# Optimization experiments

Measured on AMD Instinct MI355X. Metric: run time of the kernel, lower is better.

## Reference

```python
import jax, jax.numpy as jnp
import numpy as np

STRIDE = (1, 1, 1)  # (h_stride, w_stride, d_stride)
# padding order in module: (left,right,up,down,forward,backward) -> h, w, d dims
PAD = ((1, 1), (1, 1), (1, 1))  # ((pad_left,pad_right) on h, (up,down) on w, (fwd,bwd) on d)


def setup_inputs() -> dict:
    key = jax.random.key(0)
    k1, k2, k3 = jax.random.split(key, 3)
    X = jax.random.normal(k1, (4, 32, 32, 64, 64), dtype=jnp.float32)        # (B, Cin, h, w, d)
    weight = jax.random.normal(k2, (64, 32, 3, 3, 3), dtype=jnp.float32) * 0.5  # (Cout, Cin, kh, kw, kd)
    bias = jax.random.normal(k3, (64,), dtype=jnp.float32) * 0.5
    return {"X": X, "weight": weight, "bias": bias}


def _conv3d(X, weight, bias):
    # cross-correlation conv3d, identical math to the nested-loop MAC in MyConv3d
    y = jax.lax.conv_general_dilated(
        X, weight,
        window_strides=STRIDE,
        padding=PAD,
        dimension_numbers=("NCHWD", "OIHWD", "NCHWD"),
    )
    return y + bias[None, :, None, None, None]


def reference(X, weight, bias):
    return _conv3d(X, weight, bias)
```

## Files before the change

### kernel.cpp

```cpp
#include <hip/hip_runtime.h>
#include <hip/hip_bf16.h>

typedef __attribute__((ext_vector_type(8))) short bf16x8;
typedef __attribute__((ext_vector_type(4))) float f32x4;

#define B_N   4
#define C_IN  32
#define C_OUT 64
#define S_H   32
#define S_W   64
#define S_D   64
#define HWD   (S_H * S_W * S_D)

#define WPK_USHORTS     (4 * 28 * 64 * 8)
#define WS_NEEDED       ((size_t)WPK_USHORTS * 2 + 64)

__device__ __forceinline__ ushort f2bf(float f) {
    unsigned u = __builtin_bit_cast(unsigned, f);
    unsigned r = (u + 0x7FFFu + ((u >> 16) & 1u)) >> 16;
    return (ushort)r;
}

typedef const __attribute__((address_space(1))) unsigned int* dma_gptr;
typedef __attribute__((address_space(3))) unsigned int* dma_lptr;

__device__ __forceinline__ void dma16(const void* g, void* l) {
    __builtin_amdgcn_global_load_lds((dma_gptr)g, (dma_lptr)l, 16, 0, 0);
}

__device__ __forceinline__ void pin_load(float& dst, const float* p) {
    asm volatile("global_load_dword %0, %1, off" : "=v"(dst) : "v"(p));
}

__global__ __launch_bounds__(256) void pack_w_kernel(
    const float* __restrict__ Wt, ushort* __restrict__ Wpk, float* __restrict__ Zpf)
{
    int idx = blockIdx.x * 256 + threadIdx.x;
    int cic = idx / 1792;
    int r   = idx - cic * 1792;
    int tap = r >> 6;
    int co  = r & 63;
    bf16x8 pk;
    #pragma unroll
    for (int j = 0; j < 8; ++j)
        pk[j] = (tap < 27) ? (short)f2bf(Wt[((long)co * C_IN + cic * 8 + j) * 27 + tap])
                           : (short)0;
    *((bf16x8*)Wpk + idx) = pk;
    if (blockIdx.x == 0 && threadIdx.x < 16) Zpf[threadIdx.x] = 0.f;
}

__global__ __launch_bounds__(256, 2) void conv3d_fused_kernel(
    const float* __restrict__ X, const ushort* __restrict__ Wpk,
    const float* __restrict__ Zpf,
    const float* __restrict__ bias, float* __restrict__ out)
{
    __shared__ ushort Xs[1188 * 8];
    __shared__ ushort Ws[1792 * 8];

    const int tid  = threadIdx.x;
    const int lane = tid & 63;
    const int wave = tid >> 6;
    const int nl   = lane & 15;
    const int quad = lane >> 4;

    const int blk = blockIdx.x;
    const int wt  = blk & 15;
    const int h   = (blk >> 4) & 31;
    const int b   = blk >> 9;
    const int w0  = wt * 4;

    const float* xb[5];
    int adv[5];
    #pragma unroll
    for (int k = 0; k < 5; ++k) {
        int s = tid + k * 256;
        xb[k] = Zpf; adv[k] = 0;
        if (s < 1188) {
            int hh   = s / 396;
            int r0   = s - hh * 396;
            int ww   = r0 / 66;
            int dpos = r0 - ww * 66;
            int hp  = h - 1 + hh;
            int wp2 = w0 - 1 + ww;
            int dp  = dpos - 1;
            bool ok = (unsigned)hp < S_H && (unsigned)wp2 < S_W && (unsigned)dp < S_D;
            if (ok) {
                xb[k]  = X + ((((long)b * C_IN) * S_H + hp) * S_W + wp2) * S_D + dp;
                adv[k] = HWD;
            }
        }
    }

    int a_off[7], b_off[7];
    #pragma unroll
    for (int tg = 0; tg < 7; ++tg) {
        int tap = tg * 4 + quad;
        int tb  = tap < 27 ? tap : 0;
        int kh = tb / 9;
        int r9 = tb - kh * 9;
        int kw = r9 / 3;
        int kd = r9 - kw * 3;
        a_off[tg] = (tap * 64 + nl) * 8;
        b_off[tg] = (((kh * 6 + kw + wave) * 66) + kd + nl) * 8;
    }

    float bs[16];
    #pragma unroll
    for (int mi = 0; mi < 4; ++mi)
        #pragma unroll
        for (int r = 0; r < 4; ++r)
            bs[mi * 4 + r] = bias[mi * 16 + quad * 4 + r];

    f32x4 acc[16];
    #pragma unroll
    for (int i = 0; i < 16; ++i) acc[i] = (f32x4){0.f, 0.f, 0.f, 0.f};

    float xv[5][8];

    #pragma unroll
    for (int k = 0; k < 5; ++k) {
        int s = tid + k * 256;
        if (s < 1188) {
            #pragma unroll
            for (int j = 0; j < 8; ++j)
                pin_load(xv[k][j], xb[k] + (long)j * adv[k]);
        }
    }
    __builtin_amdgcn_sched_barrier(0);
    #pragma unroll
    for (int k = 0; k < 7; ++k) {
        int s = tid + k * 256;
        dma16(Wpk + s * 8, &Ws[s * 8]);
    }
    __builtin_amdgcn_sched_barrier(0);
    asm volatile("s_waitcnt vmcnt(7)" ::: "memory");
    __builtin_amdgcn_sched_barrier(0);
    #pragma unroll
    for (int k = 0; k < 5; ++k) {
        int s = tid + k * 256;
        if (s < 1188) {
            bf16x8 pk;
            #pragma unroll
            for (int j = 0; j < 8; ++j) pk[j] = (short)f2bf(xv[k][j]);
            *(bf16x8*)&Xs[s * 8] = pk;
        }
    }

    for (int cic = 0; cic < 4; ++cic) {
        __syncthreads();

        if (cic < 3) {
            #pragma unroll
            for (int k = 0; k < 5; ++k) {
                int s = tid + k * 256;
                if (s < 1188) {
                    #pragma unroll
                    for (int j = 0; j < 8; ++j)
                        pin_load(xv[k][j],
                                 xb[k] + (long)((cic + 1) * 8 + j) * adv[k]);
                }
            }
        }
        __builtin_amdgcn_sched_barrier(0);

        #pragma unroll
        for (int tg = 0; tg < 7; ++tg) {
            bf16x8 af[4], bf[4];
            #pragma unroll
            for (int mi = 0; mi < 4; ++mi)
                af[mi] = *(const bf16x8*)&Ws[a_off[tg] + mi * 128];
            #pragma unroll
            for (int dt = 0; dt < 4; ++dt)
                bf[dt] = *(const bf16x8*)&Xs[b_off[tg] + dt * 128];
            #pragma unroll
            for (int mi = 0; mi < 4; ++mi)
                #pragma unroll
                for (int dt = 0; dt < 4; ++dt)
                    acc[mi * 4 + dt] = __builtin_amdgcn_mfma_f32_16x16x32_bf16(
                        af[mi], bf[dt], acc[mi * 4 + dt], 0, 0, 0);
        }

        if (cic < 3) {
            __syncthreads();
            asm volatile("s_waitcnt vmcnt(0)" ::: "memory");
            __builtin_amdgcn_sched_barrier(0);

            {
                const ushort* src = Wpk + (long)(cic + 1) * 1792 * 8;
                #pragma unroll
                for (int k = 0; k < 7; ++k) {
                    int s = tid + k * 256;
                    dma16(src + s * 8, &Ws[s * 8]);
                }
            }
            #pragma unroll
            for (int k = 0; k < 5; ++k) {
                int s = tid + k * 256;
                if (s < 1188) {
                    bf16x8 pk;
                    #pragma unroll
                    for (int j = 0; j < 8; ++j) pk[j] = (short)f2bf(xv[k][j]);
                    *(bf16x8*)&Xs[s * 8] = pk;
                }
            }
        }
    }

    const int w = w0 + wave;
    #pragma unroll
    for (int mi = 0; mi < 4; ++mi) {
        #pragma unroll
        for (int dt = 0; dt < 4; ++dt) {
            f32x4 a = acc[mi * 4 + dt];
            int d0 = dt * 16 + nl;
            #pragma unroll
            for (int r = 0; r < 4; ++r) {
                int co = mi * 16 + quad * 4 + r;
                out[(((long)(b * C_OUT + co) * S_H + h) * S_W + w) * S_D + d0]
                    = a[r] + bs[mi * 4 + r];
            }
        }
    }
}

__global__ __launch_bounds__(256) void conv3d_mfma_fallback(
    const float* __restrict__ X, const float* __restrict__ Wt,
    const float* __restrict__ bias, float* __restrict__ out)
{
    __shared__ ushort Xs[3 * 6 * 66 * 8];
    __shared__ ushort Ws[28 * 64 * 8];

    const int tid  = threadIdx.x;
    const int lane = tid & 63;
    const int wave = tid >> 6;
    const int nl   = lane & 15;
    const int quad = lane >> 4;
    const int co_base = wave * 16;

    const int blk = blockIdx.x;
    const int wt  = blk & 15;
    const int h   = (blk >> 4) & 31;
    const int b   = blk >> 9;
    const int w0  = wt * 4;

    float bs[4];
    #pragma unroll
    for (int r = 0; r < 4; ++r) bs[r] = bias[co_base + quad * 4 + r];

    f32x4 acc[16];
    #pragma unroll
    for (int i = 0; i < 16; ++i) acc[i] = (f32x4){0.f, 0.f, 0.f, 0.f};

    for (int cic = 0; cic < 4; ++cic) {
        __syncthreads();
        for (int s = tid; s < 64 * 27; s += 256) {
            int co = s / 27;
            int t  = s - co * 27;
            const float* wp = Wt + ((long)co * C_IN + cic * 8) * 27 + t;
            bf16x8 pk;
            #pragma unroll
            for (int j = 0; j < 8; ++j) pk[j] = (short)f2bf(wp[j * 27]);
            *(bf16x8*)&Ws[(t * 64 + co) * 8] = pk;
        }
        for (int s = tid; s < 64; s += 256) {
            bf16x8 z;
            #pragma unroll
            for (int j = 0; j < 8; ++j) z[j] = 0;
            *(bf16x8*)&Ws[(27 * 64 + s) * 8] = z;
        }
        for (int s = tid; s < 1188; s += 256) {
            int hh   = s / 396;
            int r0   = s - hh * 396;
            int ww   = r0 / 66;
            int dpos = r0 - ww * 66;
            int hp = h - 1 + hh;
            int wp2 = w0 - 1 + ww;
            int dp = dpos - 1;
            bool ok = (unsigned)hp < S_H && (unsigned)wp2 < S_W && (unsigned)dp < S_D;
            int hc = min(max(hp, 0), S_H - 1);
            int wc = min(max(wp2, 0), S_W - 1);
            int dc = min(max(dp, 0), S_D - 1);
            const float* xp = X + (((long)(b * C_IN + cic * 8) * S_H + hc) * S_W + wc) * S_D + dc;
            bf16x8 pk;
            #pragma unroll
            for (int j = 0; j < 8; ++j) {
                float v = xp[(long)j * HWD];
                pk[j] = ok ? (short)f2bf(v) : (short)0;
            }
            *(bf16x8*)&Xs[s * 8] = pk;
        }
        __syncthreads();

        #pragma unroll
        for (int tg = 0; tg < 7; ++tg) {
            int tap = tg * 4 + quad;
            bf16x8 afrag = *(const bf16x8*)&Ws[(tap * 64 + co_base + nl) * 8];
            int tb = tap < 27 ? tap : 0;
            int kh = tb / 9;
            int r9 = tb - kh * 9;
            int kw = r9 / 3;
            int kd = r9 - kw * 3;
            int bbase = ((kh * 6 + kw) * 66 + kd + nl) * 8;
            #pragma unroll
            for (int wi = 0; wi < 4; ++wi) {
                #pragma unroll
                for (int dt = 0; dt < 4; ++dt) {
                    bf16x8 bfrag = *(const bf16x8*)&Xs[bbase + wi * (66 * 8) + dt * (16 * 8)];
                    acc[wi * 4 + dt] = __builtin_amdgcn_mfma_f32_16x16x32_bf16(
                        afrag, bfrag, acc[wi * 4 + dt], 0, 0, 0);
                }
            }
        }
    }

    #pragma unroll
    for (int wi = 0; wi < 4; ++wi) {
        int w = w0 + wi;
        #pragma unroll
        for (int dt = 0; dt < 4; ++dt) {
            int d0 = dt * 16 + nl;
            f32x4 a = acc[wi * 4 + dt];
            #pragma unroll
            for (int r = 0; r < 4; ++r) {
                int co = co_base + quad * 4 + r;
                out[(((long)(b * C_OUT + co) * S_H + h) * S_W + w) * S_D + d0] = a[r] + bs[r];
            }
        }
    }
}

extern "C" void kernel_launch(void* const* d_in, const int* in_sizes, int n_in,
                              void* d_out, int out_size, void* d_ws, size_t ws_size,
                              hipStream_t stream) {
    const float* X    = (const float*)d_in[0];
    const float* Wt   = (const float*)d_in[1];
    const float* bias = (const float*)d_in[2];
    float* out = (float*)d_out;

    if (ws_size >= WS_NEEDED) {
        ushort* Wpk = (ushort*)d_ws;
        float*  Zpf = (float*)((char*)d_ws + (size_t)WPK_USHORTS * 2);
        pack_w_kernel<<<dim3(28),   dim3(256), 0, stream>>>(Wt, Wpk, Zpf);
        conv3d_fused_kernel<<<dim3(2048), dim3(256), 0, stream>>>(X, Wpk, Zpf, bias, out);
    } else {
        conv3d_mfma_fallback<<<dim3(2048), dim3(256), 0, stream>>>(X, Wt, bias, out);
    }
}
```

Baseline: 224.9 us.

## Widen conv tile to 8 w-positions per block and drop prefetch pipelining

Each block now computes 8 output w-columns instead of 4, with each wave handling two w positions. This halves the grid and reduces the redundant halo loads of X per output and the per-block weight reloads. The register prefetch of the next input-channel chunk, which overlapped it with MFMA, is replaced by synchronous staging after compute. The accumulator count doubles to 32 f32x4, which raises register pressure under the 2-blocks-per-SM launch bound and risks spills or lower occupancy.

```diff
diff --git a/kernel.cpp b/kernel.cpp
--- a/kernel.cpp
+++ b/kernel.cpp
@@ -26,10 +26,6 @@
 
 __device__ __forceinline__ void dma16(const void* g, void* l) {
     __builtin_amdgcn_global_load_lds((dma_gptr)g, (dma_lptr)l, 16, 0, 0);
-}
-
-__device__ __forceinline__ void pin_load(float& dst, const float* p) {
-    asm volatile("global_load_dword %0, %1, off" : "=v"(dst) : "v"(p));
 }
 
 __global__ __launch_bounds__(256) void pack_w_kernel(
@@ -54,7 +50,7 @@
     const float* __restrict__ Zpf,
     const float* __restrict__ bias, float* __restrict__ out)
 {
-    __shared__ ushort Xs[1188 * 8];
+    __shared__ ushort Xs[1980 * 8];
     __shared__ ushort Ws[1792 * 8];
 
     const int tid  = threadIdx.x;
@@ -64,20 +60,20 @@
     const int quad = lane >> 4;
 
     const int blk = blockIdx.x;
-    const int wt  = blk & 15;
-    const int h   = (blk >> 4) & 31;
-    const int b   = blk >> 9;
-    const int w0  = wt * 4;
-
-    const float* xb[5];
-    int adv[5];
-    #pragma unroll
-    for (int k = 0; k < 5; ++k) {
+    const int wt  = blk & 7;
+    const int h   = (blk >> 3) & 31;
+    const int b   = blk >> 8;
+    const int w0  = wt * 8;
+
+    const float* xb[8];
+    int adv[8];
+    #pragma unroll
+    for (int k = 0; k < 8; ++k) {
         int s = tid + k * 256;
         xb[k] = Zpf; adv[k] = 0;
-        if (s < 1188) {
-            int hh   = s / 396;
-            int r0   = s - hh * 396;
+        if (s < 1980) {
+            int hh   = s / 660;
+            int r0   = s - hh * 660;
             int ww   = r0 / 66;
             int dpos = r0 - ww * 66;
             int hp  = h - 1 + hh;
@@ -101,7 +97,7 @@
         int kw = r9 / 3;
         int kd = r9 - kw * 3;
         a_off[tg] = (tap * 64 + nl) * 8;
-        b_off[tg] = (((kh * 6 + kw + wave) * 66) + kd + nl) * 8;
+        b_off[tg] = (((kh * 10 + wave * 2 + kw) * 66) + kd + nl) * 8;
     }
 
     float bs[16];
@@ -111,79 +107,74 @@
         for (int r = 0; r < 4; ++r)
             bs[mi * 4 + r] = bias[mi * 16 + quad * 4 + r];
 
-    f32x4 acc[16];
-    #pragma unroll
-    for (int i = 0; i < 16; ++i) acc[i] = (f32x4){0.f, 0.f, 0.f, 0.f};
-
-    float xv[5][8];
-
-    #pragma unroll
-    for (int k = 0; k < 5; ++k) {
-        int s = tid + k * 256;
-        if (s < 1188) {
-            #pragma unroll
-            for (int j = 0; j < 8; ++j)
-                pin_load(xv[k][j], xb[k] + (long)j * adv[k]);
-        }
-    }
-    __builtin_amdgcn_sched_barrier(0);
+    f32x4 acc[32];
+    #pragma unroll
+    for (int i = 0; i < 32; ++i) acc[i] = (f32x4){0.f, 0.f, 0.f, 0.f};
+
+    #define STAGE_X(cc)                                                       \
+        do {                                                                  \
+            _Pragma("unroll")                                                 \
+            for (int g = 0; g < 2; ++g) {                                     \
+                float xv[4][8];                                               \
+                _Pragma("unroll")                                             \
+                for (int k = 0; k < 4; ++k) {                                 \
+                    int kk = g * 4 + k;                                       \
+                    int s  = tid + kk * 256;                                  \
+                    if (s < 1980) {                                           \
+                        _Pragma("unroll")                                     \
+                        for (int j = 0; j < 8; ++j)                           \
+                            xv[k][j] = xb[kk][(long)((cc) * 8 + j) * adv[kk]];\
+                    }                                                         \
+                }                                                             \
+                _Pragma("unroll")                                             \
+                for (int k = 0; k < 4; ++k) {                                 \
+                    int kk = g * 4 + k;                                       \
+                    int s  = tid + kk * 256;                                  \
+                    if (s < 1980) {                                           \
+                        bf16x8 pk;                                            \
+                        _Pragma("unroll")                                     \
+                        for (int j = 0; j < 8; ++j)                           \
+                            pk[j] = (short)f2bf(xv[k][j]);                    \
+                        *(bf16x8*)&Xs[s * 8] = pk;                            \
+                    }                                                         \
+                }                                                             \
+            }                                                                 \
+        } while (0)
+
     #pragma unroll
     for (int k = 0; k < 7; ++k) {
         int s = tid + k * 256;
         dma16(Wpk + s * 8, &Ws[s * 8]);
     }
-    __builtin_amdgcn_sched_barrier(0);
-    asm volatile("s_waitcnt vmcnt(7)" ::: "memory");
-    __builtin_amdgcn_sched_barrier(0);
-    #pragma unroll
-    for (int k = 0; k < 5; ++k) {
-        int s = tid + k * 256;
-        if (s < 1188) {
-            bf16x8 pk;
-            #pragma unroll
-            for (int j = 0; j < 8; ++j) pk[j] = (short)f2bf(xv[k][j]);
-            *(bf16x8*)&Xs[s * 8] = pk;
-        }
-    }
+    STAGE_X(0);
 
     for (int cic = 0; cic < 4; ++cic) {
         __syncthreads();
 
-        if (cic < 3) {
-            #pragma unroll
-            for (int k = 0; k < 5; ++k) {
-                int s = tid + k * 256;
-                if (s < 1188) {
-                    #pragma unroll
-                    for (int j = 0; j < 8; ++j)
-                        pin_load(xv[k][j],
-                                 xb[k] + (long)((cic + 1) * 8 + j) * adv[k]);
-                }
-            }
-        }
-        __builtin_amdgcn_sched_barrier(0);
-
         #pragma unroll
         for (int tg = 0; tg < 7; ++tg) {
-            bf16x8 af[4], bf[4];
+            bf16x8 af[4];
             #pragma unroll
             for (int mi = 0; mi < 4; ++mi)
                 af[mi] = *(const bf16x8*)&Ws[a_off[tg] + mi * 128];
             #pragma unroll
-            for (int dt = 0; dt < 4; ++dt)
-                bf[dt] = *(const bf16x8*)&Xs[b_off[tg] + dt * 128];
-            #pragma unroll
-            for (int mi = 0; mi < 4; ++mi)
+            for (int wo = 0; wo < 2; ++wo) {
+                bf16x8 bf[4];
                 #pragma unroll
                 for (int dt = 0; dt < 4; ++dt)
-                    acc[mi * 4 + dt] = __builtin_amdgcn_mfma_f32_16x16x32_bf16(
-                        af[mi], bf[dt], acc[mi * 4 + dt], 0, 0, 0);
+                    bf[dt] = *(const bf16x8*)&Xs[b_off[tg] + wo * 528 + dt * 128];
+                #pragma unroll
+                for (int mi = 0; mi < 4; ++mi)
+                    #pragma unroll
+                    for (int dt = 0; dt < 4; ++dt)
+                        acc[wo * 16 + mi * 4 + dt] =
+                            __builtin_amdgcn_mfma_f32_16x16x32_bf16(
+                                af[mi], bf[dt], acc[wo * 16 + mi * 4 + dt], 0, 0, 0);
+            }
         }
 
         if (cic < 3) {
             __syncthreads();
-            asm volatile("s_waitcnt vmcnt(0)" ::: "memory");
-            __builtin_amdgcn_sched_barrier(0);
 
             {
                 const ushort* src = Wpk + (long)(cic + 1) * 1792 * 8;
@@ -193,31 +184,26 @@
                     dma16(src + s * 8, &Ws[s * 8]);
                 }
             }
-            #pragma unroll
-            for (int k = 0; k < 5; ++k) {
-                int s = tid + k * 256;
-                if (s < 1188) {
-                    bf16x8 pk;
-                    #pragma unroll
-                    for (int j = 0; j < 8; ++j) pk[j] = (short)f2bf(xv[k][j]);
-                    *(bf16x8*)&Xs[s * 8] = pk;
+            STAGE_X(cic + 1);
+        }
+    }
+    #undef STAGE_X
+
+    #pragma unroll
+    for (int wo = 0; wo < 2; ++wo) {
+        const int w = w0 + wave * 2 + wo;
+        #pragma unroll
+        for (int mi = 0; mi < 4; ++mi) {
+            #pragma unroll
+            for (int dt = 0; dt < 4; ++dt) {
+                f32x4 a = acc[wo * 16 + mi * 4 + dt];
+                int d0 = dt * 16 + nl;
+                #pragma unroll
+                for (int r = 0; r < 4; ++r) {
+                    int co = mi * 16 + quad * 4 + r;
+                    out[(((long)(b * C_OUT + co) * S_H + h) * S_W + w) * S_D + d0]
+                        = a[r] + bs[mi * 4 + r];
                 }
-            }
-        }
-    }
-
-    const int w = w0 + wave;
-    #pragma unroll
-    for (int mi = 0; mi < 4; ++mi) {
-        #pragma unroll
-        for (int dt = 0; dt < 4; ++dt) {
-            f32x4 a = acc[mi * 4 + dt];
-            int d0 = dt * 16 + nl;
-            #pragma unroll
-            for (int r = 0; r < 4; ++r) {
-                int co = mi * 16 + quad * 4 + r;
-                out[(((long)(b * C_OUT + co) * S_H + h) * S_W + w) * S_D + d0]
-                    = a[r] + bs[mi * 4 + r];
             }
         }
     }
@@ -341,7 +327,7 @@
         ushort* Wpk = (ushort*)d_ws;
         float*  Zpf = (float*)((char*)d_ws + (size_t)WPK_USHORTS * 2);
         pack_w_kernel<<<dim3(28),   dim3(256), 0, stream>>>(Wt, Wpk, Zpf);
-        conv3d_fused_kernel<<<dim3(2048), dim3(256), 0, stream>>>(X, Wpk, Zpf, bias, out);
+        conv3d_fused_kernel<<<dim3(1024), dim3(256), 0, stream>>>(X, Wpk, Zpf, bias, out);
     } else {
         conv3d_mfma_fallback<<<dim3(2048), dim3(256), 0, stream>>>(X, Wt, bias, out);
     }
```

After: 216.0 us. -3.9%, faster.
